# Kernel optimization log

Measured on AMD Instinct MI355X. Metric: run time of the kernel, lower is better.

Reference implementation:

```python
import jax, jax.numpy as jnp
import numpy as np

K = 7            # involution kernel size
G = 4            # groups = c1 // 16
GC = 16          # group_channels
BN_EPS = 1e-5


def setup_inputs() -> dict:
    key = jax.random.key(0)
    ks = jax.random.split(key, 6)
    B, C, H, W = 4, 64, 128, 128
    KO = K * K * G  # 196 output channels of the 1x1 kernel-generating conv
    return {
        "x": jax.random.normal(ks[0], (B, C, H, W), dtype=jnp.float32),
        "conv_w": jax.random.normal(ks[1], (KO, C), dtype=jnp.float32) * (1.0 / np.sqrt(C)),
        "bn_gamma": jax.random.uniform(ks[2], (KO,), dtype=jnp.float32, minval=0.5, maxval=1.5),
        "bn_beta": jax.random.normal(ks[3], (KO,), dtype=jnp.float32) * 0.1,
        "bn_mean": jax.random.normal(ks[4], (KO,), dtype=jnp.float32) * 0.1,
        "bn_var": jax.random.uniform(ks[5], (KO,), dtype=jnp.float32, minval=0.5, maxval=1.5),
    }


def reference(x, conv_w, bn_gamma, bn_beta, bn_mean, bn_var):
    B, C, H, W = x.shape
    pad = (K - 1) // 2

    # 1x1 Conv (YOLO Conv = conv + BN(eval) + SiLU) generating per-pixel kernels
    z = jnp.einsum('bchw,oc->bohw', x, conv_w)
    scale = bn_gamma / jnp.sqrt(bn_var + BN_EPS)
    z = z * scale[None, :, None, None] + (bn_beta - bn_mean * scale)[None, :, None, None]
    weight = jax.nn.silu(z)                                   # [B, G*K*K, H, W]
    weight = weight.reshape(B, G, K * K, H, W)

    # unfold: im2col patches, channel-major (c, kh, kw) like torch.nn.Unfold
    patches = jax.lax.conv_general_dilated_patches(
        x, filter_shape=(K, K), window_strides=(1, 1),
        padding=[(pad, pad), (pad, pad)],
        dimension_numbers=('NCHW', 'OIHW', 'NCHW'))            # [B, C*K*K, H, W]
    patches = patches.reshape(B, G, GC, K * K, H, W)

    # weighted sum over the K*K kernel positions
    out = jnp.einsum('bgkhw,bgckhw->bgchw', weight, patches)   # [B, G, GC, H, W]
    return out.reshape(B, C, H, W)
```

## Files before the change

kernel.cpp:

```cpp
#include <hip/hip_runtime.h>

#define B_   4
#define C_   64
#define H_   128
#define W_   128
#define KS   7
#define G_   4
#define GC_  16
#define KK   49
#define PAD  3
#define TH   8
#define TW   16
#define HW_  (H_ * W_)
#define ZKHB 2112

#define XOFF 0
#define WOFF 17408
#define SCOFF 26112
#define SBOFF 26312
#define LDSZ 26512

typedef float f32x4  __attribute__((ext_vector_type(4)));
typedef short bf16x8 __attribute__((ext_vector_type(8)));
typedef short bf16x4 __attribute__((ext_vector_type(4)));
typedef unsigned int u32x4 __attribute__((ext_vector_type(4)));
typedef __fp16 h16x2 __attribute__((ext_vector_type(2)));

__device__ __forceinline__ unsigned f2bf(float f) {
    unsigned u = __float_as_uint(f);
    unsigned r = u + 0x7FFFu + ((u >> 16) & 1u);
    return r >> 16;
}
__device__ __forceinline__ unsigned pk2(float a, float b) {
    union { h16x2 h; unsigned u; } x;
    x.h = __builtin_amdgcn_cvt_pkrtz(a, b);
    return x.u;
}
__device__ __forceinline__ h16x2 ash2(unsigned u) {
    union { unsigned u; h16x2 h; } x; x.u = u; return x.h;
}
__device__ __forceinline__ unsigned short f16b(float f) {
    union { __fp16 h; unsigned short s; } x; x.h = (__fp16)f; return x.s;
}
#if __has_builtin(__builtin_amdgcn_fdot2)
#define DOT2(a, b, c) __builtin_amdgcn_fdot2((a), (b), (c), false)
#else
#define DOT2(a, b, c) ((c) + (float)(a)[0] * (float)(b)[0] + (float)(a)[1] * (float)(b)[1])
#endif
#define AB(a, b) __builtin_amdgcn_alignbit((a), (b), 16)

#define LOADQ(S, KH_) do {                                                     \
    const int gh_  = h0 + y8 + (KH_) - PAD;                                    \
    const int ghc_ = gh_ < 0 ? 0 : (gh_ > H_ - 1 ? H_ - 1 : gh_);              \
    const float* rp_ = xc + (size_t)ghc_ * W_;                                 \
    if (ledge) {                                                               \
        const f32x4* vp_ = (const f32x4*)rp_;                                  \
        q##S##0 = vp_[0]; q##S##1 = vp_[1]; q##S##2 = vp_[2];                  \
    } else if (redge) {                                                        \
        const f32x4* vp_ = (const f32x4*)(rp_ + 116);                          \
        q##S##0 = vp_[0]; q##S##1 = vp_[1]; q##S##2 = vp_[2];                  \
    } else {                                                                   \
        const f32x4* vp_ = (const f32x4*)(rp_ + w0 + xh * 8 - 4);              \
        q##S##0 = vp_[0]; q##S##1 = vp_[1]; q##S##2 = vp_[2]; q##S##3 = vp_[3];\
    }                                                                          \
} while (0)

#define PACKD(S) do {                                                          \
    if (ledge) {                                                               \
        d##S##0 = 0u;                                                          \
        d##S##1 = pk2(0.f, q##S##0[0]);                                        \
        d##S##2 = pk2(q##S##0[1], q##S##0[2]);                                 \
        d##S##3 = pk2(q##S##0[3], q##S##1[0]);                                 \
        d##S##4 = pk2(q##S##1[1], q##S##1[2]);                                 \
        d##S##5 = pk2(q##S##1[3], q##S##2[0]);                                 \
        d##S##6 = pk2(q##S##2[1], q##S##2[2]);                                 \
    } else if (redge) {                                                        \
        d##S##0 = pk2(q##S##0[1], q##S##0[2]);                                 \
        d##S##1 = pk2(q##S##0[3], q##S##1[0]);                                 \
        d##S##2 = pk2(q##S##1[1], q##S##1[2]);                                 \
        d##S##3 = pk2(q##S##1[3], q##S##2[0]);                                 \
        d##S##4 = pk2(q##S##2[1], q##S##2[2]);                                 \
        d##S##5 = pk2(q##S##2[3], 0.f);                                        \
        d##S##6 = 0u;                                                          \
    } else {                                                                   \
        d##S##0 = pk2(q##S##0[1], q##S##0[2]);                                 \
        d##S##1 = pk2(q##S##0[3], q##S##1[0]);                                 \
        d##S##2 = pk2(q##S##1[1], q##S##1[2]);                                 \
        d##S##3 = pk2(q##S##1[3], q##S##2[0]);                                 \
        d##S##4 = pk2(q##S##2[1], q##S##2[2]);                                 \
        d##S##5 = pk2(q##S##2[3], q##S##3[0]);                                 \
        d##S##6 = pk2(q##S##3[1], q##S##3[2]);                                 \
    }                                                                          \
} while (0)

#define FMAD(S, KH_) do {                                                      \
    const int gh_ = h0 + y8 + (KH_) - PAD;                                     \
    if (gh_ >= 0 && gh_ < H_) {                                                \
        const int zo_ = (KH_) * ZKHB;                                          \
        const unsigned r0_ = AB(d##S##1, d##S##0);                             \
        const unsigned r1_ = AB(d##S##2, d##S##1);                             \
        const unsigned r2_ = AB(d##S##3, d##S##2);                             \
        const unsigned r3_ = AB(d##S##4, d##S##3);                             \
        const unsigned r4_ = AB(d##S##5, d##S##4);                             \
        const unsigned r5_ = AB(d##S##6, d##S##5);                             \
        const unsigned r6_ = AB(d##S##6, d##S##6);                             \
        u32x4 q_;                                                              \
        q_ = *(const u32x4*)(zp0 + zo_);                                       \
        a0 = DOT2(ash2(q_[0]), ash2(d##S##0), a0);                             \
        a0 = DOT2(ash2(q_[1]), ash2(d##S##1), a0);                             \
        a0 = DOT2(ash2(q_[2]), ash2(d##S##2), a0);                             \
        a0 = DOT2(ash2(q_[3]), ash2(d##S##3), a0);                             \
        q_ = *(const u32x4*)(zp1 + zo_);                                       \
        a1 = DOT2(ash2(q_[0]), ash2(r0_), a1);                                 \
        a1 = DOT2(ash2(q_[1]), ash2(r1_), a1);                                 \
        a1 = DOT2(ash2(q_[2]), ash2(r2_), a1);                                 \
        a1 = DOT2(ash2(q_[3]), ash2(r3_), a1);                                 \
        q_ = *(const u32x4*)(zp2 + zo_);                                       \
        a2 = DOT2(ash2(q_[0]), ash2(d##S##1), a2);                             \
        a2 = DOT2(ash2(q_[1]), ash2(d##S##2), a2);                             \
        a2 = DOT2(ash2(q_[2]), ash2(d##S##3), a2);                             \
        a2 = DOT2(ash2(q_[3]), ash2(d##S##4), a2);                             \
        q_ = *(const u32x4*)(zp3 + zo_);                                       \
        a3 = DOT2(ash2(q_[0]), ash2(r1_), a3);                                 \
        a3 = DOT2(ash2(q_[1]), ash2(r2_), a3);                                 \
        a3 = DOT2(ash2(q_[2]), ash2(r3_), a3);                                 \
        a3 = DOT2(ash2(q_[3]), ash2(r4_), a3);                                 \
        q_ = *(const u32x4*)(zp4 + zo_);                                       \
        a4 = DOT2(ash2(q_[0]), ash2(d##S##2), a4);                             \
        a4 = DOT2(ash2(q_[1]), ash2(d##S##3), a4);                             \
        a4 = DOT2(ash2(q_[2]), ash2(d##S##4), a4);                             \
        a4 = DOT2(ash2(q_[3]), ash2(d##S##5), a4);                             \
        q_ = *(const u32x4*)(zp5 + zo_);                                       \
        a5 = DOT2(ash2(q_[0]), ash2(r2_), a5);                                 \
        a5 = DOT2(ash2(q_[1]), ash2(r3_), a5);                                 \
        a5 = DOT2(ash2(q_[2]), ash2(r4_), a5);                                 \
        a5 = DOT2(ash2(q_[3]), ash2(r5_), a5);                                 \
        q_ = *(const u32x4*)(zp6 + zo_);                                       \
        a6 = DOT2(ash2(q_[0]), ash2(d##S##3), a6);                             \
        a6 = DOT2(ash2(q_[1]), ash2(d##S##4), a6);                             \
        a6 = DOT2(ash2(q_[2]), ash2(d##S##5), a6);                             \
        a6 = DOT2(ash2(q_[3]), ash2(d##S##6), a6);                             \
        q_ = *(const u32x4*)(zp7 + zo_);                                       \
        a7 = DOT2(ash2(q_[0]), ash2(r3_), a7);                                 \
        a7 = DOT2(ash2(q_[1]), ash2(r4_), a7);                                 \
        a7 = DOT2(ash2(q_[2]), ash2(r5_), a7);                                 \
        a7 = DOT2(ash2(q_[3]), ash2(r6_), a7);                                 \
    }                                                                          \
} while (0)

__global__ __launch_bounds__(256, 4) void invol_fused16(
    const float* __restrict__ x,
    const float* __restrict__ cw,
    const float* __restrict__ bng,
    const float* __restrict__ bnb,
    const float* __restrict__ bnm,
    const float* __restrict__ bnv,
    float* __restrict__ out)
{
    __shared__ __align__(16) char lds[LDSZ];

    const int tid  = threadIdx.x;
    const int lane = tid & 63;
    const int wv   = tid >> 6;
    const int l15  = lane & 15;
    const int l4   = lane >> 4;

    const int bid = blockIdx.x;
    const int xcd = bid & 7;
    const int s   = bid >> 3;
    const int b   = xcd >> 1;
    const int g   = (xcd & 1) * 2 + (s >> 7);
    const int by  = (s >> 3) & 15;
    const int bx  = s & 7;
    const int w0  = bx * TW;
    const int h0  = by * TH;

    const int c2 = tid >> 4;
    const int y8 = (tid >> 1) & 7;
    const int xh = tid & 1;
    const bool ledge = (bx == 0) & (xh == 0);
    const bool redge = (bx == W_ / TW - 1) & (xh == 1);
    const float* xc = x + (size_t)(b * C_ + g * GC_ + c2) * HW_;

    f32x4 qA0 = {0,0,0,0}, qA1 = {0,0,0,0}, qA2 = {0,0,0,0}, qA3 = {0,0,0,0};
    f32x4 qB0 = {0,0,0,0}, qB1 = {0,0,0,0}, qB2 = {0,0,0,0}, qB3 = {0,0,0,0};
    unsigned dA0, dA1, dA2, dA3, dA4, dA5, dA6;
    unsigned dB0, dB1, dB2, dB3, dB4, dB5, dB6;

    LOADQ(A, 0);

    {
        const float* xb = x + (size_t)b * C_ * HW_;
        const int p  = tid & 127;
        const int cb = tid >> 7;
        const float* src = xb + (size_t)cb * HW_ + (h0 + (p >> 4)) * W_ + w0 + (p & 15);
        char* dst = lds + XOFF + p * 136 + cb * 2;
#pragma unroll
        for (int it = 0; it < 32; ++it) {
            *(unsigned short*)(dst + it * 4) =
                (unsigned short)f2bf(src[(size_t)(2 * it) * HW_]);
        }
    }

    if (tid < KK) {
        const int o = g * KK + tid;
        const float scv = bng[o] * rsqrtf(bnv[o] + 1e-5f);
        *(float*)(lds + SCOFF + tid * 4) = scv;
        *(float*)(lds + SBOFF + tid * 4) = bnb[o] - bnm[o] * scv;
    }

    __syncthreads();

    {
        const float* cwg = cw + (size_t)g * KK * C_;
        const int c  = tid & 63;
        const int kb = tid >> 6;
#pragma unroll
        for (int it = 0; it < 16; ++it) {
            const int k = it * 4 + kb;
            float v = 0.f;
            if (k < KK)
                v = cwg[k * C_ + c] * *(const float*)(lds + SCOFF + k * 4);
            *(unsigned short*)(lds + WOFF + k * 136 + c * 2) = (unsigned short)f2bf(v);
        }
    }

    bf16x8 afr[2][2];
#pragma unroll
    for (int mt = 0; mt < 2; ++mt) {
        const int px = (wv * 2 + mt) * 16 + l15;
        const char* base_ = lds + XOFF + px * 136;
#pragma unroll
        for (int ks = 0; ks < 2; ++ks) {
            const char* pA = base_ + ks * 64 + l4 * 16;
            const bf16x4 lo = *(const bf16x4*)(pA);
            const bf16x4 hi = *(const bf16x4*)(pA + 8);
            bf16x8 f;
            f[0] = lo[0]; f[1] = lo[1]; f[2] = lo[2]; f[3] = lo[3];
            f[4] = hi[0]; f[5] = hi[1]; f[6] = hi[2]; f[7] = hi[3];
            afr[mt][ks] = f;
        }
    }

    __syncthreads();

    bf16x8 bfr[4][2];
#pragma unroll
    for (int nt = 0; nt < 4; ++nt) {
        const int k = nt * 16 + l15;
        const char* base_ = lds + WOFF + k * 136;
#pragma unroll
        for (int ks = 0; ks < 2; ++ks) {
            const char* pB = base_ + ks * 64 + l4 * 16;
            const bf16x4 lo = *(const bf16x4*)(pB);
            const bf16x4 hi = *(const bf16x4*)(pB + 8);
            bf16x8 f;
            f[0] = lo[0]; f[1] = lo[1]; f[2] = lo[2]; f[3] = lo[3];
            f[4] = hi[0]; f[5] = hi[1]; f[6] = hi[2]; f[7] = hi[3];
            bfr[nt][ks] = f;
        }
    }

    f32x4 acc1[2][4];
#pragma unroll
    for (int mt = 0; mt < 2; ++mt)
#pragma unroll
        for (int nt = 0; nt < 4; ++nt) {
            f32x4 a = {0.f, 0.f, 0.f, 0.f};
            a = __builtin_amdgcn_mfma_f32_16x16x32_bf16(afr[mt][0], bfr[nt][0], a, 0, 0, 0);
            a = __builtin_amdgcn_mfma_f32_16x16x32_bf16(afr[mt][1], bfr[nt][1], a, 0, 0, 0);
            acc1[mt][nt] = a;
        }

#pragma unroll
    for (int nt = 0; nt < 4; ++nt) {
        const int k = nt * 16 + l15;
        if (k < KK) {
            const int kh = (k * 9363) >> 16;
            const int kw = k - kh * 7;
            const int kbase = kh * ZKHB + kw * 2;
            const float bi = *(const float*)(lds + SBOFF + k * 4);
#pragma unroll
            for (int mt = 0; mt < 2; ++mt) {
                const int px0 = (wv * 2 + mt) * 16 + l4 * 4;
#pragma unroll
                for (int r = 0; r < 4; ++r) {
                    const int px = px0 + r;
                    const int sw = (px << 4) ^ (((px >> 3) & 7) << 4);
                    const float t = acc1[mt][nt][r] + bi;
                    const float v = __fdividef(t, 1.0f + __expf(-t));
                    *(unsigned short*)(lds + kbase + sw) = f16b(v);
                }
            }
        } else if (k < 56) {
            const int khp = k - KK;
#pragma unroll
            for (int mt = 0; mt < 2; ++mt) {
                const int px0 = (wv * 2 + mt) * 16 + l4 * 4;
#pragma unroll
                for (int r = 0; r < 4; ++r) {
                    const int px = px0 + r;
                    const int sw = (px << 4) ^ (((px >> 3) & 7) << 4);
                    *(unsigned short*)(lds + khp * ZKHB + sw + 14) = 0;
                }
            }
        }
    }

    __syncthreads();

    float a0 = 0.f, a1 = 0.f, a2 = 0.f, a3 = 0.f;
    float a4 = 0.f, a5 = 0.f, a6 = 0.f, a7 = 0.f;

    const int pxb = y8 * 16 + xh * 8;
    const int mx  = ((2 * y8 + xh) & 7) << 4;
    const char* zbase = lds + (pxb << 4);
    const char* zp0 = zbase + ((0 << 4) ^ mx);
    const char* zp1 = zbase + ((1 << 4) ^ mx);
    const char* zp2 = zbase + ((2 << 4) ^ mx);
    const char* zp3 = zbase + ((3 << 4) ^ mx);
    const char* zp4 = zbase + ((4 << 4) ^ mx);
    const char* zp5 = zbase + ((5 << 4) ^ mx);
    const char* zp6 = zbase + ((6 << 4) ^ mx);
    const char* zp7 = zbase + ((7 << 4) ^ mx);

#pragma unroll 1
    for (int kh2 = 0; kh2 < 3; ++kh2) {
        LOADQ(B, 2 * kh2 + 1);
        PACKD(A); FMAD(A, 2 * kh2);
        LOADQ(A, 2 * kh2 + 2);
        PACKD(B); FMAD(B, 2 * kh2 + 1);
    }
    PACKD(A); FMAD(A, 6);

    float* og = out + (size_t)(b * C_ + g * GC_ + c2) * HW_
                    + (h0 + y8) * W_ + w0 + xh * 8;
    {
        f32x4 v;
        v[0] = a0; v[1] = a1; v[2] = a2; v[3] = a3;
        *(f32x4*)(og + 0) = v;
        v[0] = a4; v[1] = a5; v[2] = a6; v[3] = a7;
        *(f32x4*)(og + 4) = v;
    }
}

extern "C" void kernel_launch(void* const* d_in, const int* in_sizes, int n_in,
                              void* d_out, int out_size, void* d_ws, size_t ws_size,
                              hipStream_t stream) {
    const float* x   = (const float*)d_in[0];
    const float* cw  = (const float*)d_in[1];
    const float* bng = (const float*)d_in[2];
    const float* bnb = (const float*)d_in[3];
    const float* bnm = (const float*)d_in[4];
    const float* bnv = (const float*)d_in[5];
    float* out = (float*)d_out;

    invol_fused16<<<dim3(2048), dim3(256), 0, stream>>>(x, cw, bng, bnb, bnm,
                                                        bnv, out);
}
```

Baseline: 37.82 us.

## Load MFMA A-fragments directly from global and drop the final block barrier

The LDS staging pass for the bf16 input tile is removed. Each wave now reads its A-fragments for the 1x1 kernel-generating GEMM straight from global memory, converting to bf16 in registers, which shrinks the LDS footprint. The thread-to-(row, channel) mapping is changed so each wave consumes only the generated weights for its own two pixel rows. That makes the __syncthreads before the involution accumulation unnecessary, and the first barrier becomes a bare s_barrier. The trade-off is uncoalesced, channel-strided global loads for the A fragments, plus reliance on intra-wave ordering for LDS correctness.

```diff
diff --git a/kernel.cpp b/kernel.cpp
--- a/kernel.cpp
+++ b/kernel.cpp
@@ -14,11 +14,10 @@
 #define HW_  (H_ * W_)
 #define ZKHB 2112
 
-#define XOFF 0
-#define WOFF 17408
-#define SCOFF 26112
-#define SBOFF 26312
-#define LDSZ 26512
+#define WOFF  14784
+#define SCOFF 23488
+#define SBOFF 23688
+#define LDSZ  23888
 
 typedef float f32x4  __attribute__((ext_vector_type(4)));
 typedef short bf16x8 __attribute__((ext_vector_type(8)));
@@ -148,7 +147,7 @@
     }                                                                          \
 } while (0)
 
-__global__ __launch_bounds__(256, 4) void invol_fused16(
+__global__ __launch_bounds__(256, 4) void invol_fused17(
     const float* __restrict__ x,
     const float* __restrict__ cw,
     const float* __restrict__ bng,
@@ -175,8 +174,8 @@
     const int w0  = bx * TW;
     const int h0  = by * TH;
 
-    const int c2 = tid >> 4;
-    const int y8 = (tid >> 1) & 7;
+    const int y8 = tid >> 5;
+    const int c2 = (tid >> 1) & 15;
     const int xh = tid & 1;
     const bool ledge = (bx == 0) & (xh == 0);
     const bool redge = (bx == W_ / TW - 1) & (xh == 1);
@@ -188,19 +187,6 @@
     unsigned dB0, dB1, dB2, dB3, dB4, dB5, dB6;
 
     LOADQ(A, 0);
-
-    {
-        const float* xb = x + (size_t)b * C_ * HW_;
-        const int p  = tid & 127;
-        const int cb = tid >> 7;
-        const float* src = xb + (size_t)cb * HW_ + (h0 + (p >> 4)) * W_ + w0 + (p & 15);
-        char* dst = lds + XOFF + p * 136 + cb * 2;
-#pragma unroll
-        for (int it = 0; it < 32; ++it) {
-            *(unsigned short*)(dst + it * 4) =
-                (unsigned short)f2bf(src[(size_t)(2 * it) * HW_]);
-        }
-    }
 
     if (tid < KK) {
         const int o = g * KK + tid;
@@ -208,9 +194,7 @@
         *(float*)(lds + SCOFF + tid * 4) = scv;
         *(float*)(lds + SBOFF + tid * 4) = bnb[o] - bnm[o] * scv;
     }
-
-    __syncthreads();
-
+    __builtin_amdgcn_s_barrier();
     {
         const float* cwg = cw + (size_t)g * KK * C_;
         const int c  = tid & 63;
@@ -226,19 +210,21 @@
     }
 
     bf16x8 afr[2][2];
-#pragma unroll
-    for (int mt = 0; mt < 2; ++mt) {
-        const int px = (wv * 2 + mt) * 16 + l15;
-        const char* base_ = lds + XOFF + px * 136;
-#pragma unroll
-        for (int ks = 0; ks < 2; ++ks) {
-            const char* pA = base_ + ks * 64 + l4 * 16;
-            const bf16x4 lo = *(const bf16x4*)(pA);
-            const bf16x4 hi = *(const bf16x4*)(pA + 8);
-            bf16x8 f;
-            f[0] = lo[0]; f[1] = lo[1]; f[2] = lo[2]; f[3] = lo[3];
-            f[4] = hi[0]; f[5] = hi[1]; f[6] = hi[2]; f[7] = hi[3];
-            afr[mt][ks] = f;
+    {
+        const float* xb = x + (size_t)b * C_ * HW_;
+#pragma unroll
+        for (int mt = 0; mt < 2; ++mt) {
+            const int hh = h0 + wv * 2 + mt;
+            const float* xp = xb + hh * W_ + (w0 + l15);
+#pragma unroll
+            for (int ks = 0; ks < 2; ++ks) {
+                const int c0 = ks * 32 + l4 * 8;
+                bf16x8 a;
+#pragma unroll
+                for (int j = 0; j < 8; ++j)
+                    a[j] = (short)f2bf(xp[(size_t)(c0 + j) * HW_]);
+                afr[mt][ks] = a;
+            }
         }
     }
 
@@ -307,7 +293,6 @@
         }
     }
 
-    __syncthreads();
 
     float a0 = 0.f, a1 = 0.f, a2 = 0.f, a3 = 0.f;
     float a4 = 0.f, a5 = 0.f, a6 = 0.f, a7 = 0.f;
@@ -355,6 +340,6 @@
     const float* bnv = (const float*)d_in[5];
     float* out = (float*)d_out;
 
-    invol_fused16<<<dim3(2048), dim3(256), 0, stream>>>(x, cw, bng, bnb, bnm,
+    invol_fused17<<<dim3(2048), dim3(256), 0, stream>>>(x, cw, bng, bnb, bnm,
                                                         bnv, out);
 }
```

After: 33.59 us (median of 2 runs). 11.2% less time.
